# Performance work log

Measured on AMD Instinct MI355X. Metric: run time of the kernel, lower is better.

## Reference

```python
import jax, jax.numpy as jnp
import numpy as np

C1, C2, C3, C4, C5 = 20, 100, 500, 2000, 10000
FEAT, B = 512, 8192
# parent maps (stand-ins for l1_to_l2..l4_to_l5 group lists): child c -> parent c // fanout
P5 = jnp.arange(C5) // 5   # l5 class -> l4 group
P4 = jnp.arange(C4) // 4   # l4 class -> l3 group
P3 = jnp.arange(C3) // 5   # l3 class -> l2 group
P2 = jnp.arange(C2) // 5   # l2 class -> l1 group


def _l2norm(w):
    # F.normalize(w, p=2, dim=1)
    return w / jnp.maximum(jnp.linalg.norm(w, axis=1, keepdims=True), 1e-12)


def _jsd(p, q, eps=1e-8):
    # Jensen-Shannon divergence between row-wise distributions, mean over batch
    m = 0.5 * (p + q)
    log_m = jnp.log(m + eps)
    kl_pm = jnp.sum(p * (jnp.log(p + eps) - log_m), axis=1)
    kl_qm = jnp.sum(q * (jnp.log(q + eps) - log_m), axis=1)
    return jnp.mean(0.5 * (kl_pm + kl_qm))


def setup_inputs() -> dict:
    key = jax.random.key(0)
    k = jax.random.split(key, 8)
    s = 0.02
    return {
        "x": jax.random.normal(k[0], (B, FEAT), jnp.float32),
        "targets": jax.random.randint(k[1], (B,), 0, C5, jnp.int32),
        "W1": jax.random.normal(k[2], (C1, FEAT), jnp.float32) * s,
        "b1": jnp.zeros((C1,), jnp.float32),
        "W2": jax.random.normal(k[3], (C2, FEAT), jnp.float32) * s,
        "b2": jnp.zeros((C2,), jnp.float32),
        "W3": jax.random.normal(k[4], (C3, FEAT), jnp.float32) * s,
        "b3": jnp.zeros((C3,), jnp.float32),
        "W4": jax.random.normal(k[5], (C4, FEAT), jnp.float32) * s,
        "b4": jnp.zeros((C4,), jnp.float32),
        "W5": jax.random.normal(k[6], (C5, FEAT), jnp.float32) * s,
        "b5": jnp.zeros((C5,), jnp.float32),
    }


def reference(x, targets, W1, b1, W2, b2, W3, b3, W4, b4, W5, b5):
    # row-normalized classifier weights (second F.normalize in the original is idempotent)
    w1, w2, w3, w4, w5 = (_l2norm(W1), _l2norm(W2), _l2norm(W3), _l2norm(W4), _l2norm(W5))
    l1 = x @ w1.T + b1
    l2 = x @ w2.T + b2
    l3 = x @ w3.T + b3
    l4 = x @ w4.T + b4
    l5 = x @ w5.T + b5  # [B, C5]

    # cross-entropy on finest level logits
    logp5 = jax.nn.log_softmax(l5, axis=1)
    ce_loss = -jnp.mean(jnp.take_along_axis(logp5, targets[:, None].astype(jnp.int32), axis=1)[:, 0])

    p1 = jax.nn.softmax(l1, axis=1)
    p2 = jax.nn.softmax(l2, axis=1)
    p3 = jax.nn.softmax(l3, axis=1)
    p4 = jax.nn.softmax(l4, axis=1)
    p5 = jax.nn.softmax(l5, axis=1)

    # hierarchy-aggregated weights: segment-sum child rows, renormalize, cosine vs parent
    def agg_cos(parent_w, child_w, seg, num_seg):
        hat = _l2norm(jax.ops.segment_sum(child_w, seg, num_segments=num_seg))
        return jnp.mean(jnp.sum(parent_w * hat, axis=1))  # rows are unit norm -> cosine

    l2_w_45 = agg_cos(w4, w5, P5, C4)
    l2_w_34 = agg_cos(w3, w4, P4, C3)
    l2_w_23 = agg_cos(w2, w3, P3, C2)
    l2_w_12 = agg_cos(w1, w2, P2, C1)

    # hierarchy-aggregated probabilities: column segment-sums, then JSD vs parent
    def agg_prob(child_p, seg, num_seg):
        return jax.ops.segment_sum(child_p.T, seg, num_segments=num_seg).T

    jsd_45 = _jsd(agg_prob(p5, P5, C4), p4)
    jsd_34 = _jsd(agg_prob(p4, P4, C3), p3)
    jsd_23 = _jsd(agg_prob(p3, P3, C2), p2)
    jsd_12 = _jsd(agg_prob(p2, P2, C1), p1)

    loss = ce_loss + (jsd_45 + jsd_34 + jsd_23 + jsd_12) - (l2_w_45 + l2_w_34 + l2_w_23 + l2_w_12)
    return p5, loss
```

## Files before the change

### kernel.cpp

```cpp
#include <hip/hip_runtime.h>
#include <hip/hip_bf16.h>
#include <stdint.h>

typedef unsigned short u16;
typedef __bf16 bf16x8 __attribute__((ext_vector_type(8)));
typedef float f32x4 __attribute__((ext_vector_type(4)));
typedef unsigned int u32x4 __attribute__((ext_vector_type(4)));

#define FEAT 512
#define BATCH 8192
#define NC1 20
#define NC2 100
#define NC3 500
#define NC4 2000
#define NC5 10000
#define NCAT 2620
#define LDP 2624
#define NTOT 12620
#define NCT 40
#define WN_BLOCKS 3155
#define CAST_BLOCKS 2048
#define NGRP 2620
#define WCOS_BLOCKS 655

__device__ inline u16 f2bf(float f) {
    unsigned int u = __builtin_bit_cast(unsigned int, f);
    unsigned int r = (u + 0x7FFFu + ((u >> 16) & 1u)) >> 16;
    return (u16)r;
}
__device__ inline float bfu(u16 u) {
    return __builtin_bit_cast(float, (unsigned int)u << 16);
}

__device__ inline float waveReduceSum(float v) {
    #pragma unroll
    for (int off = 32; off > 0; off >>= 1) v += __shfl_xor(v, off);
    return v;
}
__device__ inline float waveReduceMax(float v) {
    #pragma unroll
    for (int off = 32; off > 0; off >>= 1) v = fmaxf(v, __shfl_xor(v, off));
    return v;
}
__device__ inline float blockReduceSum(float v, float* sh) {
    int t = threadIdx.x;
    v = waveReduceSum(v);
    __syncthreads();
    if ((t & 63) == 0) sh[t >> 6] = v;
    __syncthreads();
    return sh[0] + sh[1] + sh[2] + sh[3];
}
__device__ inline float blockReduceMax(float v, float* sh) {
    int t = threadIdx.x;
    v = waveReduceMax(v);
    __syncthreads();
    if ((t & 63) == 0) sh[t >> 6] = v;
    __syncthreads();
    return fmaxf(fmaxf(sh[0], sh[1]), fmaxf(sh[2], sh[3]));
}

__device__ inline void gload16(const void* g, void* l) {
    __builtin_amdgcn_global_load_lds((const __attribute__((address_space(1))) void*)g,
                                     (__attribute__((address_space(3))) void*)l, 16, 0, 0);
}


__global__ __launch_bounds__(256) void prep(const float* __restrict__ x, u16* __restrict__ xb,
                                            const float* __restrict__ W1, const float* __restrict__ b1,
                                            const float* __restrict__ W2, const float* __restrict__ b2,
                                            const float* __restrict__ W3, const float* __restrict__ b3,
                                            const float* __restrict__ W4, const float* __restrict__ b4,
                                            const float* __restrict__ W5, const float* __restrict__ b5,
                                            u16* __restrict__ wb, float* __restrict__ biascat,
                                            float* __restrict__ c45, float* __restrict__ c34,
                                            float* __restrict__ c23, float* __restrict__ c12) {
    int bid = blockIdx.x;
    if (bid < WN_BLOCKS) {
        int r = bid * 4 + (threadIdx.x >> 6);
        if (r >= NTOT) return;
        int t = threadIdx.x & 63;
        const float* W; const float* b; int lr;
        if      (r < 20)   { W = W1; b = b1; lr = r; }
        else if (r < 120)  { W = W2; b = b2; lr = r - 20; }
        else if (r < 620)  { W = W3; b = b3; lr = r - 120; }
        else if (r < 2620) { W = W4; b = b4; lr = r - 620; }
        else               { W = W5; b = b5; lr = r - 2620; }
        const float* p = W + (size_t)lr * FEAT + t * 8;
        float v[8]; float ss = 0.f;
        #pragma unroll
        for (int j = 0; j < 8; ++j) { v[j] = p[j]; ss += v[j] * v[j]; }
        ss = waveReduceSum(ss);
        float inv = 1.0f / fmaxf(sqrtf(ss), 1e-12f);
        union { u16 u[8]; uint4 q; } o;
        #pragma unroll
        for (int j = 0; j < 8; ++j) o.u[j] = f2bf(v[j] * inv);
        ((uint4*)(wb + (size_t)r * FEAT))[t] = o.q;
        if (t == 0) biascat[r] = b[lr];
    } else if (bid < WN_BLOCKS + CAST_BLOCKS) {
        int i = (bid - WN_BLOCKS) * 256 + threadIdx.x;
        const float* p = x + (size_t)i * 8;
        union { u16 u[8]; uint4 v; } o;
        #pragma unroll
        for (int j = 0; j < 8; ++j) o.u[j] = f2bf(p[j]);
        ((uint4*)xb)[i] = o.v;
    } else {
        int g = (bid - WN_BLOCKS - CAST_BLOCKS) * 4 + (threadIdx.x >> 6);
        if (g >= NGRP) return;
        int t = threadIdx.x & 63;
        const float* Wp; const float* Wc; int fan, j; float* dst;
        if      (g < 2000) { Wp = W4; Wc = W5; fan = 5; dst = c45; j = g; }
        else if (g < 2500) { Wp = W3; Wc = W4; fan = 4; dst = c34; j = g - 2000; }
        else if (g < 2600) { Wp = W2; Wc = W3; fan = 5; dst = c23; j = g - 2500; }
        else               { Wp = W1; Wc = W2; fan = 5; dst = c12; j = g - 2600; }

        float hat[8] = {0, 0, 0, 0, 0, 0, 0, 0};
        for (int c = 0; c < fan; ++c) {
            const float* cr = Wc + ((size_t)(j * fan + c)) * FEAT + t * 8;
            float v[8]; float ss = 0.f;
            #pragma unroll
            for (int i = 0; i < 8; ++i) { v[i] = cr[i]; ss += v[i] * v[i]; }
            ss = waveReduceSum(ss);
            float inv = 1.0f / fmaxf(sqrtf(ss), 1e-12f);
            #pragma unroll
            for (int i = 0; i < 8; ++i) hat[i] += v[i] * inv;
        }
        float hs = 0.f;
        #pragma unroll
        for (int i = 0; i < 8; ++i) hs += hat[i] * hat[i];
        hs = waveReduceSum(hs);
        float hinv = 1.0f / fmaxf(sqrtf(hs), 1e-12f);
        const float* pr = Wp + (size_t)j * FEAT + t * 8;
        float ps = 0.f, dot = 0.f;
        #pragma unroll
        for (int i = 0; i < 8; ++i) { float pv = pr[i]; ps += pv * pv; dot += pv * hat[i]; }
        ps = waveReduceSum(ps);
        dot = waveReduceSum(dot);
        if (t == 0) dst[j] = dot * hinv / fmaxf(sqrtf(ps), 1e-12f);
    }
}


#define BM 256
#define BN 256
#define BK 64
#define KITERS (FEAT / BK)

__global__ __launch_bounds__(512, 2) void gemm_all(const u16* __restrict__ A, const u16* __restrict__ Bw,
                                                   const float* __restrict__ bias,
                                                   u16* __restrict__ pcat, u16* __restrict__ l5b,
                                                   float* __restrict__ pmax, float* __restrict__ psum) {
    __shared__ u16 sAB[2][2 * BM * BK];
    const int t = threadIdx.x;
    const int lane = t & 63, wid = t >> 6;
    const int lane15 = lane & 15, q = lane >> 4;
    const int wr = wid >> 2, wcol = wid & 3;

    int nwg = gridDim.x * gridDim.y;
    int lid = blockIdx.y * gridDim.x + blockIdx.x;
    int cpx = nwg >> 3;
    int swz = (lid & 7) * cpx + (lid >> 3);
    int bx = swz % gridDim.x, by = swz / gridDim.x;
    const int r0 = bx * BM, c0 = by * BN;

    f32x4 acc[8][4];
    #pragma unroll
    for (int m = 0; m < 8; ++m)
        #pragma unroll
        for (int n = 0; n < 4; ++n) acc[m][n] = f32x4{0.f, 0.f, 0.f, 0.f};

    auto stage = [&](int kt, int buf) {
        char* base = (char*)sAB[buf];
        #pragma unroll
        for (int p = 0; p < 8; ++p) {
            int chunk = p * 512 + t;
            int row = chunk >> 3, blk = chunk & 7;
            int srck = 8 * (blk ^ (row & 7));
            const u16* g;
            if (p < 4) {
                g = A + (size_t)(r0 + row) * FEAT + kt + srck;
            } else {
                int brow = c0 + (row - 256); if (brow >= NTOT) brow = NTOT - 1;
                g = Bw + (size_t)brow * FEAT + kt + srck;
            }
            gload16(g, base + (size_t)chunk * 16);
        }
    };

    stage(0, 0);
    stage(BK, 1);
    for (int ki = 0; ki < KITERS; ++ki) {
        if (ki + 1 < KITERS) { asm volatile("s_waitcnt vmcnt(8)" ::: "memory"); }
        else                 { asm volatile("s_waitcnt vmcnt(0)" ::: "memory"); }
        __builtin_amdgcn_sched_barrier(0);
        __builtin_amdgcn_s_barrier();
        __builtin_amdgcn_sched_barrier(0);
        char* sAb = (char*)sAB[ki & 1];
        char* sBb = sAb + BM * BK * 2;
        #pragma unroll
        for (int ks = 0; ks < 2; ++ks) {
            const int kko = ks * 4 + q;
            bf16x8 af[8], bv[4];
            #pragma unroll
            for (int m = 0; m < 8; ++m) {
                int row = wr * 128 + m * 16 + lane15;
                af[m] = *reinterpret_cast<const bf16x8*>(sAb + row * 128 + 16 * (kko ^ (row & 7)));
            }
            #pragma unroll
            for (int n = 0; n < 4; ++n) {
                int row = wcol * 64 + n * 16 + lane15;
                bv[n] = *reinterpret_cast<const bf16x8*>(sBb + row * 128 + 16 * (kko ^ (row & 7)));
            }
            __builtin_amdgcn_s_setprio(1);
            #pragma unroll
            for (int m = 0; m < 8; ++m)
                #pragma unroll
                for (int n = 0; n < 4; ++n)
                    acc[m][n] = __builtin_amdgcn_mfma_f32_16x16x32_bf16(bv[n], af[m], acc[m][n], 0, 0, 0);
            __builtin_amdgcn_s_setprio(0);
        }
        __builtin_amdgcn_sched_barrier(0);
        __builtin_amdgcn_s_barrier();
        __builtin_amdgcn_sched_barrier(0);
        if (ki + 2 < KITERS) stage((ki + 2) * BK, ki & 1);
    }

    bool vld[4], svld[4]; int cb[4];
    #pragma unroll
    for (int n = 0; n < 4; ++n) {
        cb[n] = c0 + wcol * 64 + n * 16 + q * 4;
        vld[n] = (cb[n] < NTOT);
        svld[n] = vld[n] && (cb[n] >= NCAT);
        if (vld[n]) {
            float b0 = bias[cb[n]], b1 = bias[cb[n] + 1], b2 = bias[cb[n] + 2], b3 = bias[cb[n] + 3];
            #pragma unroll
            for (int m = 0; m < 8; ++m) {
                acc[m][n][0] += b0; acc[m][n][1] += b1;
                acc[m][n][2] += b2; acc[m][n][3] += b3;
            }
        }
    }

    if (by >= 10) {
        float* fmx = (float*)sAB;
        float* fsm = fmx + 1024;
        float bm[8];
        #pragma unroll
        for (int m = 0; m < 8; ++m) {
            float v = -1e30f;
            #pragma unroll
            for (int n = 0; n < 4; ++n)
                if (svld[n]) {
                    #pragma unroll
                    for (int j = 0; j < 4; ++j) v = fmaxf(v, acc[m][n][j]);
                }
            v = fmaxf(v, __shfl_xor(v, 16));
            v = fmaxf(v, __shfl_xor(v, 32));
            bm[m] = v;
        }
        if (lane < 16) {
            #pragma unroll
            for (int m = 0; m < 8; ++m)
                fmx[(wr * 128 + m * 16 + lane15) * 4 + wcol] = bm[m];
        }
        __syncthreads();
        #pragma unroll
        for (int m = 0; m < 8; ++m) {
            int row = wr * 128 + m * 16 + lane15;
            bm[m] = fmaxf(fmaxf(fmx[row * 4], fmx[row * 4 + 1]),
                          fmaxf(fmx[row * 4 + 2], fmx[row * 4 + 3]));
        }
        float sm[8];
        #pragma unroll
        for (int m = 0; m < 8; ++m) {
            float s = 0.f;
            #pragma unroll
            for (int n = 0; n < 4; ++n)
                if (svld[n]) {
                    #pragma unroll
                    for (int j = 0; j < 4; ++j) s += __expf(acc[m][n][j] - bm[m]);
                }
            s += __shfl_xor(s, 16);
            s += __shfl_xor(s, 32);
            sm[m] = s;
        }
        if (lane < 16) {
            #pragma unroll
            for (int m = 0; m < 8; ++m)
                fsm[(wr * 128 + m * 16 + lane15) * 4 + wcol] = sm[m];
        }
        __syncthreads();
        if (t < 256) {
            float m4 = fmaxf(fmaxf(fmx[t * 4], fmx[t * 4 + 1]), fmaxf(fmx[t * 4 + 2], fmx[t * 4 + 3]));
            float s4 = fsm[t * 4] + fsm[t * 4 + 1] + fsm[t * 4 + 2] + fsm[t * 4 + 3];
            size_t idx = (size_t)(r0 + t) * NCT + (by - 10);
            pmax[idx] = m4;
            psum[idx] = s4;
        }
    }

    #pragma unroll
    for (int m = 0; m < 8; ++m) {
        int row = r0 + wr * 128 + m * 16 + lane15;
        #pragma unroll
        for (int n = 0; n < 4; ++n) {
            if (vld[n]) {
                union { u16 u[4]; uint2 v; } pk;
                #pragma unroll
                for (int j = 0; j < 4; ++j) pk.u[j] = f2bf(acc[m][n][j]);
                u16* dst = (cb[n] < NCAT)
                    ? &pcat[(size_t)row * LDP + cb[n]]
                    : &l5b[(size_t)row * NC5 + (cb[n] - NCAT)];
                *reinterpret_cast<uint2*>(dst) = pk.v;
            }
        }
    }
}


__global__ __launch_bounds__(256) void probs_all(const u16* __restrict__ l5b, float* __restrict__ out,
                                                 const u16* __restrict__ pcat,
                                                 const float* __restrict__ pmax, const float* __restrict__ psum,
                                                 const int* __restrict__ tgt,
                                                 float* __restrict__ cerow,
                                                 float* __restrict__ j12, float* __restrict__ j23,
                                                 float* __restrict__ j34, float* __restrict__ j45) {
    __shared__ u16 P5[NC5];
    __shared__ float PC[LDP];
    __shared__ float sh[4];
    __shared__ float shls;
    int b = blockIdx.x, t = threadIdx.x;
    float* orow = out + (size_t)b * NC5;
    const u16* lrow = l5b + (size_t)b * NC5;
    const u16* prow = pcat + (size_t)b * LDP;

    if (t < 64) {
        float pm = (t < NCT) ? pmax[(size_t)b * NCT + t] : -1e30f;
        float ps = (t < NCT) ? psum[(size_t)b * NCT + t] : 0.f;
        float gm = waveReduceMax(pm);
        float s = waveReduceSum(ps * __expf(pm - gm));
        if (t == 0) {
            float ls = gm + __logf(s);
            shls = ls;
            int tg = tgt[b];
            cerow[b] = -(bfu(lrow[tg]) - ls);
        }
    }
    for (int c = t; c < LDP / 8; c += 256) {
        u32x4 raw = __builtin_nontemporal_load(&((const u32x4*)prow)[c]);
        const u16* rp = (const u16*)&raw;
        #pragma unroll
        for (int k = 0; k < 8; ++k) PC[c * 8 + k] = bfu(rp[k]);
    }
    __syncthreads();
    float ls = shls;

    for (int c = t; c < NC5 / 8; c += 256) {
        u32x4 raw = __builtin_nontemporal_load(&((const u32x4*)lrow)[c]);
        const u16* rp = (const u16*)&raw;
        f32x4 p0, p1;
        #pragma unroll
        for (int k = 0; k < 4; ++k) p0[k] = __expf(bfu(rp[k]) - ls);
        #pragma unroll
        for (int k = 0; k < 4; ++k) p1[k] = __expf(bfu(rp[4 + k]) - ls);
        __builtin_nontemporal_store(p0, &((f32x4*)orow)[c * 2]);
        __builtin_nontemporal_store(p1, &((f32x4*)orow)[c * 2 + 1]);
        union { u16 u[8]; uint4 v; } pk;
        #pragma unroll
        for (int k = 0; k < 4; ++k) pk.u[k] = f2bf(p0[k]);
        #pragma unroll
        for (int k = 0; k < 4; ++k) pk.u[4 + k] = f2bf(p1[k]);
        ((uint4*)P5)[c] = pk.v;
    }
    __syncthreads();

    auto softmax_seg = [&](int off, int C) {
        float m = -1e30f;
        for (int c = t; c < C; c += 256) m = fmaxf(m, PC[off + c]);
        m = blockReduceMax(m, sh);
        float s = 0.f;
        for (int c = t; c < C; c += 256) { float e = __expf(PC[off + c] - m); PC[off + c] = e; s += e; }
        s = blockReduceSum(s, sh);
        float inv = 1.0f / s;
        for (int c = t; c < C; c += 256) PC[off + c] *= inv;
    };
    softmax_seg(0, NC1);
    softmax_seg(20, NC2);
    softmax_seg(120, NC3);
    softmax_seg(620, NC4);
    __syncthreads();

    {
        float klpm = 0.f, klqm = 0.f;
        for (int g = t; g < NC4; g += 256) {
            float qv = 0.f;
            #pragma unroll
            for (int f = 0; f < 5; ++f) qv += bfu(P5[5 * g + f]);
            float pp = PC[620 + g];
            float mm = 0.5f * (qv + pp);
            float lm = __logf(mm + 1e-8f);
            klpm += qv * (__logf(qv + 1e-8f) - lm);
            klqm += pp * (__logf(pp + 1e-8f) - lm);
        }
        float tot = blockReduceSum(0.5f * (klpm + klqm), sh);
        if (t == 0) j45[b] = tot;
    }
    auto jsd_seg = [&](int childOff, int fan, int parentOff, int nPar, float* dst) {
        float klpm = 0.f, klqm = 0.f;
        for (int g = t; g < nPar; g += 256) {
            float qv = 0.f;
            for (int f = 0; f < fan; ++f) qv += PC[childOff + g * fan + f];
            float pp = PC[parentOff + g];
            float mm = 0.5f * (qv + pp);
            float lm = __logf(mm + 1e-8f);
            klpm += qv * (__logf(qv + 1e-8f) - lm);
            klqm += pp * (__logf(pp + 1e-8f) - lm);
        }
        float tot = blockReduceSum(0.5f * (klpm + klqm), sh);
        if (t == 0) dst[b] = tot;
    };
    jsd_seg(620, 4, 120, NC3, j34);
    jsd_seg(120, 5, 20, NC2, j23);
    jsd_seg(20, 5, 0, NC1, j12);
}

__global__ __launch_bounds__(256) void finalize(const float* __restrict__ ce, const float* __restrict__ j45,
                                                const float* __restrict__ j34, const float* __restrict__ j23,
                                                const float* __restrict__ j12, const float* __restrict__ c45,
                                                const float* __restrict__ c34, const float* __restrict__ c23,
                                                const float* __restrict__ c12, float* __restrict__ lossOut) {
    __shared__ float sh[4];
    auto meanArr = [&](const float* a, int n) {
        float s = 0.f;
        for (int i = threadIdx.x; i < n; i += 256) s += a[i];
        s = blockReduceSum(s, sh);
        return s / n;
    };
    float loss = meanArr(ce, BATCH);
    loss += meanArr(j45, BATCH) + meanArr(j34, BATCH) + meanArr(j23, BATCH) + meanArr(j12, BATCH);
    loss -= meanArr(c45, NC4) + meanArr(c34, NC3) + meanArr(c23, NC2) + meanArr(c12, NC1);
    if (threadIdx.x == 0) *lossOut = loss;
}


extern "C" void kernel_launch(void* const* d_in, const int* in_sizes, int n_in,
                              void* d_out, int out_size, void* d_ws, size_t ws_size,
                              hipStream_t stream) {
    const float* x  = (const float*)d_in[0];
    const int*   tg = (const int*)d_in[1];
    const float* W1 = (const float*)d_in[2];  const float* b1 = (const float*)d_in[3];
    const float* W2 = (const float*)d_in[4];  const float* b2 = (const float*)d_in[5];
    const float* W3 = (const float*)d_in[6];  const float* b3 = (const float*)d_in[7];
    const float* W4 = (const float*)d_in[8];  const float* b4 = (const float*)d_in[9];
    const float* W5 = (const float*)d_in[10]; const float* b5 = (const float*)d_in[11];
    float* out = (float*)d_out;

    char* ws = (char*)d_ws;
    size_t off = 0;
    auto alloc = [&](size_t bytes) { void* p = ws + off; off = (off + bytes + 255) & ~(size_t)255; return p; };
    u16*   xb      = (u16*)alloc((size_t)BATCH * FEAT * 2);
    u16*   wb      = (u16*)alloc((size_t)NTOT * FEAT * 2);
    float* biascat = (float*)alloc((size_t)NTOT * 4);
    u16*   pcat    = (u16*)alloc((size_t)BATCH * LDP * 2);
    u16*   l5b     = (u16*)alloc((size_t)BATCH * NC5 * 2);
    float* pmax    = (float*)alloc((size_t)BATCH * NCT * 4);
    float* psum    = (float*)alloc((size_t)BATCH * NCT * 4);
    float* cerow   = (float*)alloc((size_t)BATCH * 4);
    float* j45     = (float*)alloc((size_t)BATCH * 4);
    float* j34     = (float*)alloc((size_t)BATCH * 4);
    float* j23     = (float*)alloc((size_t)BATCH * 4);
    float* j12     = (float*)alloc((size_t)BATCH * 4);
    float* c45     = (float*)alloc((size_t)NC4 * 4);
    float* c34     = (float*)alloc((size_t)NC3 * 4);
    float* c23     = (float*)alloc((size_t)NC2 * 4);
    float* c12     = (float*)alloc((size_t)NC1 * 4);

    prep<<<WN_BLOCKS + CAST_BLOCKS + WCOS_BLOCKS, 256, 0, stream>>>(
        x, xb, W1, b1, W2, b2, W3, b3, W4, b4, W5, b5, wb, biascat, c45, c34, c23, c12);

    gemm_all<<<dim3(BATCH / BM, (NTOT + BN - 1) / BN), 512, 0, stream>>>(
        xb, wb, biascat, pcat, l5b, pmax, psum);

    probs_all<<<BATCH, 256, 0, stream>>>(l5b, out, pcat, pmax, psum, tg, cerow,
                                         j12, j23, j34, j45);

    finalize<<<1, 256, 0, stream>>>(cerow, j45, j34, j23, j12, c45, c34, c23, c12,
                                    out + (size_t)BATCH * NC5);
}
```

Measured before the change: 390.1 us.

## Restructure GEMM main loop into half-K stages with interleaved global prefetch

Splits each K tile into two 32-wide halves stored in separate LDS regions with a new 4-way swizzle. Global loads for the next tile are issued in quarters between the MFMA groups, so memory traffic overlaps compute within one iteration instead of a coarse two-tile prefetch. A-fragment reads are split into two groups of four to cut register pressure. A __syncthreads is added before the softmax epilogue reuses the shared buffer, since loads are now in flight up to the last iteration.

Measured after the change: 395.3 us. About the same (+1.3%).

```diff
diff --git a/kernel.cpp b/kernel.cpp
--- a/kernel.cpp
+++ b/kernel.cpp
@@ -168,60 +168,116 @@
         #pragma unroll
         for (int n = 0; n < 4; ++n) acc[m][n] = f32x4{0.f, 0.f, 0.f, 0.f};
 
-    auto stage = [&](int kt, int buf) {
-        char* base = (char*)sAB[buf];
-        #pragma unroll
-        for (int p = 0; p < 8; ++p) {
-            int chunk = p * 512 + t;
-            int row = chunk >> 3, blk = chunk & 7;
-            int srck = 8 * (blk ^ (row & 7));
+    auto stageHalf = [&](char* nb, int region, int kh, int ktB) {
+        #pragma unroll
+        for (int p = 0; p < 2; ++p) {
+            int c = p * 512 + t;
+            int row = c >> 2;
+            int srck = ktB + kh * 32 + 8 * ((c & 3) ^ ((c >> 3) & 3));
             const u16* g;
-            if (p < 4) {
-                g = A + (size_t)(r0 + row) * FEAT + kt + srck;
+            if (region == 0) {
+                g = A + (size_t)(r0 + row) * FEAT + srck;
             } else {
-                int brow = c0 + (row - 256); if (brow >= NTOT) brow = NTOT - 1;
-                g = Bw + (size_t)brow * FEAT + kt + srck;
+                int br = c0 + row; if (br >= NTOT) br = NTOT - 1;
+                g = Bw + (size_t)br * FEAT + srck;
             }
-            gload16(g, base + (size_t)chunk * 16);
+            gload16(g, nb + region * 32768 + kh * 16384 + (size_t)c * 16);
         }
     };
 
-    stage(0, 0);
-    stage(BK, 1);
-    for (int ki = 0; ki < KITERS; ++ki) {
-        if (ki + 1 < KITERS) { asm volatile("s_waitcnt vmcnt(8)" ::: "memory"); }
-        else                 { asm volatile("s_waitcnt vmcnt(0)" ::: "memory"); }
+    auto readA = [&](char* sb, int ks, int mh, bf16x8* af) {
+        #pragma unroll
+        for (int i = 0; i < 4; ++i) {
+            int row = wr * 128 + (mh * 4 + i) * 16 + lane15;
+            af[i] = *reinterpret_cast<const bf16x8*>(sb + ks * 16384 + row * 64 +
+                                                     16 * ((q ^ (row >> 1)) & 3));
+        }
+    };
+    auto readB = [&](char* sb, int ks, bf16x8* bv) {
+        #pragma unroll
+        for (int n = 0; n < 4; ++n) {
+            int row = wcol * 64 + n * 16 + lane15;
+            bv[n] = *reinterpret_cast<const bf16x8*>(sb + 32768 + ks * 16384 + row * 64 +
+                                                     16 * ((q ^ (row >> 1)) & 3));
+        }
+    };
+
+    {
+        char* nb = (char*)sAB[0];
+        stageHalf(nb, 0, 0, 0);
+        stageHalf(nb, 1, 0, 0);
+        stageHalf(nb, 0, 1, 0);
+        stageHalf(nb, 1, 1, 0);
+    }
+
+    for (int T = 0; T < KITERS; ++T) {
+        char* sb = (char*)sAB[T & 1];
+        char* nb = (char*)sAB[(T + 1) & 1];
+        const bool more = (T + 1 < KITERS);
+        const int ktB = (T + 1) * BK;
+
+        asm volatile("s_waitcnt vmcnt(4)" ::: "memory");
         __builtin_amdgcn_sched_barrier(0);
         __builtin_amdgcn_s_barrier();
         __builtin_amdgcn_sched_barrier(0);
-        char* sAb = (char*)sAB[ki & 1];
-        char* sBb = sAb + BM * BK * 2;
-        #pragma unroll
-        for (int ks = 0; ks < 2; ++ks) {
-            const int kko = ks * 4 + q;
-            bf16x8 af[8], bv[4];
-            #pragma unroll
-            for (int m = 0; m < 8; ++m) {
-                int row = wr * 128 + m * 16 + lane15;
-                af[m] = *reinterpret_cast<const bf16x8*>(sAb + row * 128 + 16 * (kko ^ (row & 7)));
-            }
-            #pragma unroll
-            for (int n = 0; n < 4; ++n) {
-                int row = wcol * 64 + n * 16 + lane15;
-                bv[n] = *reinterpret_cast<const bf16x8*>(sBb + row * 128 + 16 * (kko ^ (row & 7)));
-            }
+        {
+            bf16x8 bv[4], af[4];
+            readB(sb, 0, bv);
+            readA(sb, 0, 0, af);
+            if (more) stageHalf(nb, 0, 0, ktB);
+            __builtin_amdgcn_sched_barrier(0);
             __builtin_amdgcn_s_setprio(1);
             #pragma unroll
-            for (int m = 0; m < 8; ++m)
+            for (int i = 0; i < 4; ++i)
                 #pragma unroll
                 for (int n = 0; n < 4; ++n)
-                    acc[m][n] = __builtin_amdgcn_mfma_f32_16x16x32_bf16(bv[n], af[m], acc[m][n], 0, 0, 0);
+                    acc[i][n] = __builtin_amdgcn_mfma_f32_16x16x32_bf16(bv[n], af[i], acc[i][n], 0, 0, 0);
             __builtin_amdgcn_s_setprio(0);
-        }
+            __builtin_amdgcn_sched_barrier(0);
+            readA(sb, 0, 1, af);
+            if (more) stageHalf(nb, 1, 0, ktB);
+            __builtin_amdgcn_sched_barrier(0);
+            __builtin_amdgcn_s_setprio(1);
+            #pragma unroll
+            for (int i = 0; i < 4; ++i)
+                #pragma unroll
+                for (int n = 0; n < 4; ++n)
+                    acc[4 + i][n] = __builtin_amdgcn_mfma_f32_16x16x32_bf16(bv[n], af[i], acc[4 + i][n], 0, 0, 0);
+            __builtin_amdgcn_s_setprio(0);
+            __builtin_amdgcn_sched_barrier(0);
+        }
+
+        if (more) { asm volatile("s_waitcnt vmcnt(4)" ::: "memory"); }
+        else      { asm volatile("s_waitcnt vmcnt(0)" ::: "memory"); }
         __builtin_amdgcn_sched_barrier(0);
         __builtin_amdgcn_s_barrier();
         __builtin_amdgcn_sched_barrier(0);
-        if (ki + 2 < KITERS) stage((ki + 2) * BK, ki & 1);
+        {
+            bf16x8 bv[4], af[4];
+            readB(sb, 1, bv);
+            readA(sb, 1, 0, af);
+            if (more) stageHalf(nb, 0, 1, ktB);
+            __builtin_amdgcn_sched_barrier(0);
+            __builtin_amdgcn_s_setprio(1);
+            #pragma unroll
+            for (int i = 0; i < 4; ++i)
+                #pragma unroll
+                for (int n = 0; n < 4; ++n)
+                    acc[i][n] = __builtin_amdgcn_mfma_f32_16x16x32_bf16(bv[n], af[i], acc[i][n], 0, 0, 0);
+            __builtin_amdgcn_s_setprio(0);
+            __builtin_amdgcn_sched_barrier(0);
+            readA(sb, 1, 1, af);
+            if (more) stageHalf(nb, 1, 1, ktB);
+            __builtin_amdgcn_sched_barrier(0);
+            __builtin_amdgcn_s_setprio(1);
+            #pragma unroll
+            for (int i = 0; i < 4; ++i)
+                #pragma unroll
+                for (int n = 0; n < 4; ++n)
+                    acc[4 + i][n] = __builtin_amdgcn_mfma_f32_16x16x32_bf16(bv[n], af[i], acc[4 + i][n], 0, 0, 0);
+            __builtin_amdgcn_s_setprio(0);
+            __builtin_amdgcn_sched_barrier(0);
+        }
     }
 
     bool vld[4], svld[4]; int cb[4];
@@ -257,6 +313,7 @@
             v = fmaxf(v, __shfl_xor(v, 32));
             bm[m] = v;
         }
+        __syncthreads();
         if (lane < 16) {
             #pragma unroll
             for (int m = 0; m < 8; ++m)
```
